# Optimization experiments

Measured on AMD Instinct MI355X. Metric: run time of the kernel, lower is better.

Reference implementation:

```python
import jax, jax.numpy as jnp
import numpy as np

N = 100000
E = 1600000
IN_C, HID_C, OUT_C = 64, 64, 16


def setup_inputs() -> dict:
    key = jax.random.key(0)
    k1, k2, k3, k4, k5 = jax.random.split(key, 5)
    x = jax.random.normal(k1, (N, IN_C), dtype=jnp.float32)
    edge_index = jax.random.randint(k2, (2, E), 0, N, dtype=jnp.int64)
    # Glorot-style init like PyG GCNConv
    W1 = jax.random.normal(k3, (IN_C, HID_C), dtype=jnp.float32) * (1.0 / np.sqrt(IN_C))
    b1 = jnp.zeros((HID_C,), dtype=jnp.float32)
    W2 = jax.random.normal(k4, (HID_C, OUT_C), dtype=jnp.float32) * (1.0 / np.sqrt(HID_C))
    b2 = jnp.zeros((OUT_C,), dtype=jnp.float32)
    return {"x": x, "edge_index": edge_index, "W1": W1, "b1": b1, "W2": W2, "b2": b2}


def _gcn_conv(h, src, dst, norm, W, b, n_nodes):
    # h: [N, F_in] -> linear transform first (PyG order), then normalized aggregation
    h = h @ W  # [N, F_out]
    msgs = h[src] * norm[:, None]          # gather + scale, [E+N, F_out]
    out = jax.ops.segment_sum(msgs, dst, num_segments=n_nodes)  # scatter-add
    return out + b


def reference(x, edge_index, W1, b1, W2, b2):
    n = x.shape[0]
    loop = jnp.arange(n, dtype=edge_index.dtype)
    src = jnp.concatenate([edge_index[0], loop])  # add self-loops
    dst = jnp.concatenate([edge_index[1], loop])
    # symmetric normalization D^{-1/2} (A+I) D^{-1/2}
    deg = jax.ops.segment_sum(jnp.ones_like(dst, dtype=x.dtype), dst, num_segments=n)
    dinv = jnp.where(deg > 0, jax.lax.rsqrt(deg), 0.0)
    norm = dinv[src] * dinv[dst]  # [E+N]

    h = jax.nn.relu(_gcn_conv(x, src, dst, norm, W1, b1, n))
    # dropout is identity in eval mode
    return _gcn_conv(h, src, dst, norm, W2, b2, n)
```

## Files before the change

kernel.cpp:

```cpp
#include <hip/hip_runtime.h>


namespace {
constexpr int BLK = 256;
constexpr int NPB = 256;
constexpr int PCHUNK = 8192;
constexpr int STRIDE = 5120;
constexpr int CPAD = 32;

__device__ inline float bf2f(unsigned short h) {
    union { unsigned u; float f; } v; v.u = (unsigned)h << 16; return v.f;
}
__device__ inline unsigned short f2bf(float f) {
    union { float f; unsigned u; } v; v.f = f;
    unsigned r = (v.u + 0x7FFFu + ((v.u >> 16) & 1u)) >> 16;
    return (unsigned short)r;
}
__device__ inline unsigned pack2bf(float a, float b) {
    return (unsigned)f2bf(a) | ((unsigned)f2bf(b) << 16);
}
__device__ inline int sel4(int s0, int s1, int s2, int s3, int q) {
    int sa = (q & 1) ? s1 : s0;
    int sb = (q & 1) ? s3 : s2;
    return (q & 2) ? sb : sa;
}

__device__ inline float gather8(const unsigned short* __restrict__ hhat,
                                const int* __restrict__ ssrc,
                                const float* __restrict__ dinv,
                                int base, int lane) {
    int s0 = ssrc[base + 0], s1 = ssrc[base + 1];
    int s2 = ssrc[base + 2], s3 = ssrc[base + 3];
    int s4 = ssrc[base + 4], s5 = ssrc[base + 5];
    int s6 = ssrc[base + 6], s7 = ssrc[base + 7];
    float d0 = dinv[s0], d1 = dinv[s1], d2 = dinv[s2], d3 = dinv[s3];
    float d4 = dinv[s4], d5 = dinv[s5], d6 = dinv[s6], d7 = dinv[s7];
    float v0 = bf2f(hhat[((size_t)s0 << 6) + lane]);
    float v1 = bf2f(hhat[((size_t)s1 << 6) + lane]);
    float v2 = bf2f(hhat[((size_t)s2 << 6) + lane]);
    float v3 = bf2f(hhat[((size_t)s3 << 6) + lane]);
    float v4 = bf2f(hhat[((size_t)s4 << 6) + lane]);
    float v5 = bf2f(hhat[((size_t)s5 << 6) + lane]);
    float v6 = bf2f(hhat[((size_t)s6 << 6) + lane]);
    float v7 = bf2f(hhat[((size_t)s7 << 6) + lane]);
    float t0 = fmaf(d1, v1, d0 * v0);
    float t1 = fmaf(d3, v3, d2 * v2);
    float t2 = fmaf(d5, v5, d4 * v4);
    float t3 = fmaf(d7, v7, d6 * v6);
    return (t0 + t1) + (t2 + t3);
}
__device__ inline float gather4(const unsigned short* __restrict__ hhat,
                                const int* __restrict__ ssrc,
                                const float* __restrict__ dinv,
                                int base, int lane) {
    int s0 = ssrc[base + 0], s1 = ssrc[base + 1];
    int s2 = ssrc[base + 2], s3 = ssrc[base + 3];
    float d0 = dinv[s0], d1 = dinv[s1], d2 = dinv[s2], d3 = dinv[s3];
    float v0 = bf2f(hhat[((size_t)s0 << 6) + lane]);
    float v1 = bf2f(hhat[((size_t)s1 << 6) + lane]);
    float v2 = bf2f(hhat[((size_t)s2 << 6) + lane]);
    float v3 = bf2f(hhat[((size_t)s3 << 6) + lane]);
    float t0 = fmaf(d1, v1, d0 * v0);
    float t1 = fmaf(d3, v3, d2 * v2);
    return t0 + t1;
}

__global__ __launch_bounds__(BLK) void k_part(const int* __restrict__ src,
                                              const int* __restrict__ dst,
                                              int* __restrict__ bcnt,
                                              unsigned* __restrict__ packed,
                                              int e, int nb) {
    __shared__ int hist[1024];
    __shared__ int base[1024];
    int t = threadIdx.x;
    int chunk0 = blockIdx.x * PCHUNK;
    if (chunk0 >= e) return;
    int lim = min(PCHUNK, e - chunk0);
    int lim4 = lim >> 2;
    for (int i = t; i < nb; i += BLK) hist[i] = 0;
    __syncthreads();
    const int4* d4 = (const int4*)(dst + chunk0);
    for (int i = t; i < lim4; i += BLK) {
        int4 d = d4[i];
        atomicAdd(&hist[d.x >> 8], 1);
        atomicAdd(&hist[d.y >> 8], 1);
        atomicAdd(&hist[d.z >> 8], 1);
        atomicAdd(&hist[d.w >> 8], 1);
    }
    for (int i = (lim4 << 2) + t; i < lim; i += BLK)
        atomicAdd(&hist[dst[chunk0 + i] >> 8], 1);
    __syncthreads();
    for (int i = t; i < nb; i += BLK) {
        int c = hist[i];
        base[i] = c ? (i * STRIDE + atomicAdd(&bcnt[i * CPAD], c)) : 0;
        hist[i] = 0;
    }
    __syncthreads();
    const int4* s4 = (const int4*)(src + chunk0);
    for (int i = t; i < lim4; i += BLK) {
        int4 d = d4[i];
        int4 s = s4[i];
        int b0 = d.x >> 8, b1 = d.y >> 8, b2 = d.z >> 8, b3 = d.w >> 8;
        int r0 = atomicAdd(&hist[b0], 1);
        packed[base[b0] + r0] = ((unsigned)s.x << 8) | (unsigned)(d.x & 255);
        int r1 = atomicAdd(&hist[b1], 1);
        packed[base[b1] + r1] = ((unsigned)s.y << 8) | (unsigned)(d.y & 255);
        int r2 = atomicAdd(&hist[b2], 1);
        packed[base[b2] + r2] = ((unsigned)s.z << 8) | (unsigned)(d.z & 255);
        int r3 = atomicAdd(&hist[b3], 1);
        packed[base[b3] + r3] = ((unsigned)s.w << 8) | (unsigned)(d.w & 255);
    }
    for (int i = (lim4 << 2) + t; i < lim; i += BLK) {
        int d = dst[chunk0 + i];
        int b = d >> 8;
        int r = atomicAdd(&hist[b], 1);
        packed[base[b] + r] = ((unsigned)src[chunk0 + i] << 8) | (unsigned)(d & 255);
    }
}

union SMemU {
    struct { unsigned sp[STRIDE]; int cnt[NPB]; int offs[NPB]; } s;
    float W[64 * 64];
};

__global__ __launch_bounds__(BLK) void k_sortgemm(
    const unsigned* __restrict__ packed, const int* __restrict__ bcnt,
    int* __restrict__ ssrc, int* __restrict__ rowbeg, int* __restrict__ rowcnt,
    float* __restrict__ dinv, int n, int nsort,
    const float* __restrict__ x, const float* __restrict__ W1,
    unsigned short* __restrict__ hhat, int ntiles) {
    __shared__ SMemU sm;
    int t = threadIdx.x;
    if ((int)blockIdx.x < nsort) {
        int bid = blockIdx.x;
        int b = bid >> 2;
        int qr = bid & 3;
        int regionBase = b * STRIDE;
        int ecnt = bcnt[b * CPAD];
        sm.s.cnt[t] = 0;
        __syncthreads();
        for (int i = t; i < ecnt; i += BLK) {
            unsigned p = packed[regionBase + i];
            sm.s.sp[i] = p;
            atomicAdd(&sm.s.cnt[p & 255u], 1);
        }
        __syncthreads();
        int v = sm.s.cnt[t];
        sm.s.offs[t] = v;
        __syncthreads();
        for (int off = 1; off < NPB; off <<= 1) {
            int xx = (t >= off) ? sm.s.offs[t - off] : 0;
            __syncthreads();
            sm.s.offs[t] += xx;
            __syncthreads();
        }
        int myoff = sm.s.offs[t] - v;
        int node = (b << 8) + t;
        if ((t >> 6) == qr && node < n) {
            rowbeg[node] = regionBase + myoff;
            rowcnt[node] = v;
            dinv[node] = rsqrtf((float)(v + 1));
        }
        __syncthreads();
        sm.s.cnt[t] = regionBase + myoff;
        __syncthreads();
        int lo = qr << 6, hi = lo + 64;
        for (int i = t; i < ecnt; i += BLK) {
            unsigned p = sm.s.sp[i];
            int dl = (int)(p & 255u);
            if (dl >= lo && dl < hi) {
                int pos = atomicAdd(&sm.s.cnt[dl], 1);
                ssrc[pos] = (int)(p >> 8);
            }
        }
    } else {
        #pragma unroll
        for (int i = 0; i < 16; ++i) sm.W[t + BLK * i] = W1[t + BLK * i];
        __syncthreads();
        const int cg = t & 3;
        const int ng = t >> 2;
        const float* Wc = sm.W + cg * 16;
        const int g1grid = gridDim.x - nsort;

        for (int tile = blockIdx.x - nsort; tile < ntiles; tile += g1grid) {
            const int node0 = tile * 256 + ng * 4;
            int nd[4];
            #pragma unroll
            for (int i = 0; i < 4; ++i) {
                int vv = node0 + i;
                nd[i] = (vv < n) ? vv : (n - 1);
            }
            float4 acc[4][4];
            #pragma unroll
            for (int i = 0; i < 4; ++i)
                #pragma unroll
                for (int c = 0; c < 4; ++c) acc[i][c] = make_float4(0.f, 0.f, 0.f, 0.f);

            for (int k4 = 0; k4 < 16; ++k4) {
                float4 xv[4];
                #pragma unroll
                for (int i = 0; i < 4; ++i)
                    xv[i] = ((const float4*)(x + (size_t)nd[i] * 64))[k4];
                #pragma unroll
                for (int kk = 0; kk < 4; ++kk) {
                    const float4* wr = (const float4*)(Wc + (k4 * 4 + kk) * 64);
                    float4 w0 = wr[0], w1 = wr[1], w2 = wr[2], w3 = wr[3];
                    #pragma unroll
                    for (int i = 0; i < 4; ++i) {
                        float xa[4] = {xv[i].x, xv[i].y, xv[i].z, xv[i].w};
                        float xs = xa[kk];
                        acc[i][0].x = fmaf(xs, w0.x, acc[i][0].x);
                        acc[i][0].y = fmaf(xs, w0.y, acc[i][0].y);
                        acc[i][0].z = fmaf(xs, w0.z, acc[i][0].z);
                        acc[i][0].w = fmaf(xs, w0.w, acc[i][0].w);
                        acc[i][1].x = fmaf(xs, w1.x, acc[i][1].x);
                        acc[i][1].y = fmaf(xs, w1.y, acc[i][1].y);
                        acc[i][1].z = fmaf(xs, w1.z, acc[i][1].z);
                        acc[i][1].w = fmaf(xs, w1.w, acc[i][1].w);
                        acc[i][2].x = fmaf(xs, w2.x, acc[i][2].x);
                        acc[i][2].y = fmaf(xs, w2.y, acc[i][2].y);
                        acc[i][2].z = fmaf(xs, w2.z, acc[i][2].z);
                        acc[i][2].w = fmaf(xs, w2.w, acc[i][2].w);
                        acc[i][3].x = fmaf(xs, w3.x, acc[i][3].x);
                        acc[i][3].y = fmaf(xs, w3.y, acc[i][3].y);
                        acc[i][3].z = fmaf(xs, w3.z, acc[i][3].z);
                        acc[i][3].w = fmaf(xs, w3.w, acc[i][3].w);
                    }
                }
            }
            #pragma unroll
            for (int i = 0; i < 4; ++i) {
                int vv = node0 + i;
                if (vv < n) {
                    unsigned u0 = pack2bf(acc[i][0].x, acc[i][0].y);
                    unsigned u1 = pack2bf(acc[i][0].z, acc[i][0].w);
                    unsigned u2 = pack2bf(acc[i][1].x, acc[i][1].y);
                    unsigned u3 = pack2bf(acc[i][1].z, acc[i][1].w);
                    unsigned u4 = pack2bf(acc[i][2].x, acc[i][2].y);
                    unsigned u5 = pack2bf(acc[i][2].z, acc[i][2].w);
                    unsigned u6 = pack2bf(acc[i][3].x, acc[i][3].y);
                    unsigned u7 = pack2bf(acc[i][3].z, acc[i][3].w);
                    uint4* dstp = (uint4*)(hhat + (size_t)vv * 64 + cg * 16);
                    dstp[0] = make_uint4(u0, u1, u2, u3);
                    dstp[1] = make_uint4(u4, u5, u6, u7);
                }
            }
        }
    }
}


__global__ __launch_bounds__(BLK) void k_agg1(const unsigned short* __restrict__ hhat,
                                              const int* __restrict__ rowbeg,
                                              const int* __restrict__ rowcnt,
                                              const int* __restrict__ ssrc,
                                              const float* __restrict__ dinv,
                                              const float* __restrict__ b1,
                                              const float* __restrict__ W2,
                                              unsigned short* __restrict__ h2hat, int n) {
    int pair = __builtin_amdgcn_readfirstlane(
        (int)((blockIdx.x * BLK + threadIdx.x) >> 6));
    int lane = threadIdx.x & 63;
    int wid0 = pair << 1;
    if (wid0 >= n) return;
    int wid1 = wid0 + 1;
    bool has1 = (wid1 < n);
    const int g = lane >> 4;
    const int j = lane & 15;
    float w2r[16];
    #pragma unroll
    for (int k = 0; k < 16; ++k) w2r[k] = W2[(g * 16 + k) * 16 + j];

    int beg0 = rowbeg[wid0], cnt0 = rowcnt[wid0];
    int beg1 = 0, cnt1 = 0;
    if (has1) { beg1 = rowbeg[wid1]; cnt1 = rowcnt[wid1]; }
    float a0 = dinv[wid0] * bf2f(hhat[((size_t)wid0 << 6) + lane]);
    float a1 = 0.f;
    if (has1) a1 = dinv[wid1] * bf2f(hhat[((size_t)wid1 << 6) + lane]);
    int e0 = 0, e1 = 0;
    while (e0 + 8 <= cnt0 && e1 + 8 <= cnt1) {
        float r0 = gather8(hhat, ssrc, dinv, beg0 + e0, lane);
        float r1 = gather8(hhat, ssrc, dinv, beg1 + e1, lane);
        a0 += r0;
        a1 += r1;
        e0 += 8; e1 += 8;
    }
    for (; e0 + 8 <= cnt0; e0 += 8) a0 += gather8(hhat, ssrc, dinv, beg0 + e0, lane);
    for (; e1 + 8 <= cnt1; e1 += 8) a1 += gather8(hhat, ssrc, dinv, beg1 + e1, lane);
    if (e0 + 4 <= cnt0) { a0 += gather4(hhat, ssrc, dinv, beg0 + e0, lane); e0 += 4; }
    if (e1 + 4 <= cnt1) { a1 += gather4(hhat, ssrc, dinv, beg1 + e1, lane); e1 += 4; }
    for (; e0 < cnt0; ++e0) {
        int s = ssrc[beg0 + e0];
        a0 = fmaf(dinv[s], bf2f(hhat[((size_t)s << 6) + lane]), a0);
    }
    for (; e1 < cnt1; ++e1) {
        int s = ssrc[beg1 + e1];
        a1 = fmaf(dinv[s], bf2f(hhat[((size_t)s << 6) + lane]), a1);
    }

    {
        float dv = dinv[wid0];
        float h = fmaxf(fmaf(dv, a0, b1[lane]), 0.f);
        float part = 0.f;
        #pragma unroll
        for (int k = 0; k < 16; ++k)
            part = fmaf(__shfl(h, g * 16 + k, 64), w2r[k], part);
        part += __shfl_xor(part, 16, 64);
        part += __shfl_xor(part, 32, 64);
        if (g == 0) h2hat[(size_t)wid0 * 16 + j] = f2bf(part * dv);
    }
    if (has1) {
        float dv = dinv[wid1];
        float h = fmaxf(fmaf(dv, a1, b1[lane]), 0.f);
        float part = 0.f;
        #pragma unroll
        for (int k = 0; k < 16; ++k)
            part = fmaf(__shfl(h, g * 16 + k, 64), w2r[k], part);
        part += __shfl_xor(part, 16, 64);
        part += __shfl_xor(part, 32, 64);
        if (g == 0) h2hat[(size_t)wid1 * 16 + j] = f2bf(part * dv);
    }
}

__global__ __launch_bounds__(BLK) void k_agg2(const unsigned short* __restrict__ h2,
                                              const int* __restrict__ rowbeg,
                                              const int* __restrict__ rowcnt,
                                              const int* __restrict__ ssrc,
                                              const float* __restrict__ dinv,
                                              const float* __restrict__ b2,
                                              float* __restrict__ out, int n) {
    int pair = __builtin_amdgcn_readfirstlane(
        (int)((blockIdx.x * BLK + threadIdx.x) >> 6));
    int lane = threadIdx.x & 63;
    int w0 = pair << 1;
    if (w0 >= n) return;
    int w1 = w0 + 1;
    bool has1 = (w1 < n);
    int q = lane >> 4;
    int c = lane & 15;
    int beg0 = rowbeg[w0], cnt0 = rowcnt[w0];
    int beg1 = 0, cnt1 = 0;
    if (has1) { beg1 = rowbeg[w1]; cnt1 = rowcnt[w1]; }
    float a0 = 0.f, a1 = 0.f;
    int e0 = 0, e1 = 0;
    while (e0 + 8 <= cnt0 && e1 + 8 <= cnt1) {
        int p0 = beg0 + e0, p1 = beg1 + e1;
        int x0 = ssrc[p0 + 0], x1 = ssrc[p0 + 1], x2 = ssrc[p0 + 2], x3 = ssrc[p0 + 3];
        int x4 = ssrc[p0 + 4], x5 = ssrc[p0 + 5], x6 = ssrc[p0 + 6], x7 = ssrc[p0 + 7];
        int y0 = ssrc[p1 + 0], y1 = ssrc[p1 + 1], y2 = ssrc[p1 + 2], y3 = ssrc[p1 + 3];
        int y4 = ssrc[p1 + 4], y5 = ssrc[p1 + 5], y6 = ssrc[p1 + 6], y7 = ssrc[p1 + 7];
        int sA0 = sel4(x0, x1, x2, x3, q), sB0 = sel4(x4, x5, x6, x7, q);
        int sA1 = sel4(y0, y1, y2, y3, q), sB1 = sel4(y4, y5, y6, y7, q);
        float vA0 = bf2f(h2[((size_t)sA0 << 4) + c]);
        float vB0 = bf2f(h2[((size_t)sB0 << 4) + c]);
        float vA1 = bf2f(h2[((size_t)sA1 << 4) + c]);
        float vB1 = bf2f(h2[((size_t)sB1 << 4) + c]);
        a0 += vA0 + vB0;
        a1 += vA1 + vB1;
        e0 += 8; e1 += 8;
    }
    for (; e0 + 8 <= cnt0; e0 += 8) {
        int p0 = beg0 + e0;
        int x0 = ssrc[p0 + 0], x1 = ssrc[p0 + 1], x2 = ssrc[p0 + 2], x3 = ssrc[p0 + 3];
        int x4 = ssrc[p0 + 4], x5 = ssrc[p0 + 5], x6 = ssrc[p0 + 6], x7 = ssrc[p0 + 7];
        int sA = sel4(x0, x1, x2, x3, q), sB = sel4(x4, x5, x6, x7, q);
        a0 += bf2f(h2[((size_t)sA << 4) + c]) + bf2f(h2[((size_t)sB << 4) + c]);
    }
    if (e0 + 4 <= cnt0) {
        int p0 = beg0 + e0;
        int x0 = ssrc[p0 + 0], x1 = ssrc[p0 + 1], x2 = ssrc[p0 + 2], x3 = ssrc[p0 + 3];
        a0 += bf2f(h2[((size_t)sel4(x0, x1, x2, x3, q) << 4) + c]);
        e0 += 4;
    }
    if (e0 + q < cnt0)
        a0 += bf2f(h2[((size_t)ssrc[beg0 + e0 + q] << 4) + c]);
    for (; e1 + 8 <= cnt1; e1 += 8) {
        int p1 = beg1 + e1;
        int y0 = ssrc[p1 + 0], y1 = ssrc[p1 + 1], y2 = ssrc[p1 + 2], y3 = ssrc[p1 + 3];
        int y4 = ssrc[p1 + 4], y5 = ssrc[p1 + 5], y6 = ssrc[p1 + 6], y7 = ssrc[p1 + 7];
        int sA = sel4(y0, y1, y2, y3, q), sB = sel4(y4, y5, y6, y7, q);
        a1 += bf2f(h2[((size_t)sA << 4) + c]) + bf2f(h2[((size_t)sB << 4) + c]);
    }
    if (has1 && e1 + 4 <= cnt1) {
        int p1 = beg1 + e1;
        int y0 = ssrc[p1 + 0], y1 = ssrc[p1 + 1], y2 = ssrc[p1 + 2], y3 = ssrc[p1 + 3];
        a1 += bf2f(h2[((size_t)sel4(y0, y1, y2, y3, q) << 4) + c]);
        e1 += 4;
    }
    if (has1 && e1 + q < cnt1)
        a1 += bf2f(h2[((size_t)ssrc[beg1 + e1 + q] << 4) + c]);

    a0 += __shfl_xor(a0, 16, 64);
    a0 += __shfl_xor(a0, 32, 64);
    a1 += __shfl_xor(a1, 16, 64);
    a1 += __shfl_xor(a1, 32, 64);
    if (q == 0) {
        float self0 = bf2f(h2[((size_t)w0 << 4) + c]);
        out[((size_t)w0 << 4) + c] = fmaf(dinv[w0], a0 + self0, b2[c]);
        if (has1) {
            float self1 = bf2f(h2[((size_t)w1 << 4) + c]);
            out[((size_t)w1 << 4) + c] = fmaf(dinv[w1], a1 + self1, b2[c]);
        }
    }
}

}

extern "C" void kernel_launch(void* const* d_in, const int* in_sizes, int n_in,
                              void* d_out, int out_size, void* d_ws, size_t ws_size,
                              hipStream_t stream) {
    const float* x  = (const float*)d_in[0];
    const int*   ei = (const int*)d_in[1];
    const float* W1 = (const float*)d_in[2];
    const float* b1 = (const float*)d_in[3];
    const float* W2 = (const float*)d_in[4];
    const float* b2 = (const float*)d_in[5];
    float* out = (float*)d_out;

    const int N = in_sizes[0] / 64;
    const int E = in_sizes[1] / 2;
    const int* src = ei;
    const int* dst = ei + E;
    const int nb = (N + NPB - 1) / NPB;

    char* ws = (char*)d_ws;
    size_t off = 0;
    auto alloc = [&](size_t bytes) -> char* {
        char* p = ws + off;
        off = (off + bytes + 255) & ~(size_t)255;
        return p;
    };
    int*            bcnt   = (int*)alloc((size_t)1024 * CPAD * 4);
    int*            rowbeg = (int*)alloc((size_t)N * 4);
    int*            rowcnt = (int*)alloc((size_t)N * 4);
    float*          dinv   = (float*)alloc((size_t)N * 4);
    unsigned*       packed = (unsigned*)alloc((size_t)nb * STRIDE * 4);
    int*            ssrc   = (int*)alloc((size_t)nb * STRIDE * 4);
    unsigned short* hhat   = (unsigned short*)alloc((size_t)N * 64 * 2);
    unsigned short* h2hat  = (unsigned short*)alloc((size_t)N * 16 * 2);

    const int ntiles = (N + 255) / 256;
    const int g1grid = (ntiles < 1024) ? ntiles : 1024;
    const int nchunks = (E + PCHUNK - 1) / PCHUNK;
    const int npairs = (N + 1) / 2;
    const int nb_p = (int)(((long long)npairs * 64 + BLK - 1) / BLK);
    const int nsort = nb * 4;

    const int zn = nb * CPAD;
    hipMemsetAsync(bcnt, 0, (size_t)zn * 4, stream);
    k_part<<<nchunks, BLK, 0, stream>>>(src, dst, bcnt, packed, E, nb);
    k_sortgemm<<<nsort + g1grid, BLK, 0, stream>>>(packed, bcnt, ssrc, rowbeg,
                                                   rowcnt, dinv, N, nsort,
                                                   x, W1, hhat, ntiles);
    k_agg1<<<nb_p, BLK, 0, stream>>>(hhat, rowbeg, rowcnt, ssrc, dinv, b1, W2,
                                     h2hat, N);
    k_agg2<<<nb_p, BLK, 0, stream>>>(h2hat, rowbeg, rowcnt, ssrc, dinv, b2, out, N);
}
```

Before: 217.9 us.

## Prescale layer-1 features by source dinv to drop per-edge dinv gathers

Computes node in-degrees with global atomics during partitioning, so the GEMM stage can fold dinv[src] into the bf16 hhat rows before they are stored. Layer-1 aggregation then becomes a plain sum of gathered rows, with no per-edge random dinv load and multiply. The cost is an extra global atomic per edge in k_part and a larger memset, and dinv is now applied before bf16 rounding, which slightly changes numerics. The GEMM blocks share a launch with the sort blocks, so deg must be complete before that launch.

```diff
diff --git a/kernel.cpp b/kernel.cpp
--- a/kernel.cpp
+++ b/kernel.cpp
@@ -26,15 +26,11 @@
 }
 
 __device__ inline float gather8(const unsigned short* __restrict__ hhat,
-                                const int* __restrict__ ssrc,
-                                const float* __restrict__ dinv,
-                                int base, int lane) {
+                                const int* __restrict__ ssrc, int base, int lane) {
     int s0 = ssrc[base + 0], s1 = ssrc[base + 1];
     int s2 = ssrc[base + 2], s3 = ssrc[base + 3];
     int s4 = ssrc[base + 4], s5 = ssrc[base + 5];
     int s6 = ssrc[base + 6], s7 = ssrc[base + 7];
-    float d0 = dinv[s0], d1 = dinv[s1], d2 = dinv[s2], d3 = dinv[s3];
-    float d4 = dinv[s4], d5 = dinv[s5], d6 = dinv[s6], d7 = dinv[s7];
     float v0 = bf2f(hhat[((size_t)s0 << 6) + lane]);
     float v1 = bf2f(hhat[((size_t)s1 << 6) + lane]);
     float v2 = bf2f(hhat[((size_t)s2 << 6) + lane]);
@@ -43,31 +39,23 @@
     float v5 = bf2f(hhat[((size_t)s5 << 6) + lane]);
     float v6 = bf2f(hhat[((size_t)s6 << 6) + lane]);
     float v7 = bf2f(hhat[((size_t)s7 << 6) + lane]);
-    float t0 = fmaf(d1, v1, d0 * v0);
-    float t1 = fmaf(d3, v3, d2 * v2);
-    float t2 = fmaf(d5, v5, d4 * v4);
-    float t3 = fmaf(d7, v7, d6 * v6);
-    return (t0 + t1) + (t2 + t3);
+    return ((v0 + v1) + (v2 + v3)) + ((v4 + v5) + (v6 + v7));
 }
 __device__ inline float gather4(const unsigned short* __restrict__ hhat,
-                                const int* __restrict__ ssrc,
-                                const float* __restrict__ dinv,
-                                int base, int lane) {
+                                const int* __restrict__ ssrc, int base, int lane) {
     int s0 = ssrc[base + 0], s1 = ssrc[base + 1];
     int s2 = ssrc[base + 2], s3 = ssrc[base + 3];
-    float d0 = dinv[s0], d1 = dinv[s1], d2 = dinv[s2], d3 = dinv[s3];
     float v0 = bf2f(hhat[((size_t)s0 << 6) + lane]);
     float v1 = bf2f(hhat[((size_t)s1 << 6) + lane]);
     float v2 = bf2f(hhat[((size_t)s2 << 6) + lane]);
     float v3 = bf2f(hhat[((size_t)s3 << 6) + lane]);
-    float t0 = fmaf(d1, v1, d0 * v0);
-    float t1 = fmaf(d3, v3, d2 * v2);
-    return t0 + t1;
+    return (v0 + v1) + (v2 + v3);
 }
 
 __global__ __launch_bounds__(BLK) void k_part(const int* __restrict__ src,
                                               const int* __restrict__ dst,
                                               int* __restrict__ bcnt,
+                                              int* __restrict__ deg,
                                               unsigned* __restrict__ packed,
                                               int e, int nb) {
     __shared__ int hist[1024];
@@ -86,9 +74,16 @@
         atomicAdd(&hist[d.y >> 8], 1);
         atomicAdd(&hist[d.z >> 8], 1);
         atomicAdd(&hist[d.w >> 8], 1);
-    }
-    for (int i = (lim4 << 2) + t; i < lim; i += BLK)
-        atomicAdd(&hist[dst[chunk0 + i] >> 8], 1);
+        atomicAdd(&deg[d.x], 1);
+        atomicAdd(&deg[d.y], 1);
+        atomicAdd(&deg[d.z], 1);
+        atomicAdd(&deg[d.w], 1);
+    }
+    for (int i = (lim4 << 2) + t; i < lim; i += BLK) {
+        int d = dst[chunk0 + i];
+        atomicAdd(&hist[d >> 8], 1);
+        atomicAdd(&deg[d], 1);
+    }
     __syncthreads();
     for (int i = t; i < nb; i += BLK) {
         int c = hist[i];
@@ -128,6 +123,7 @@
     int* __restrict__ ssrc, int* __restrict__ rowbeg, int* __restrict__ rowcnt,
     float* __restrict__ dinv, int n, int nsort,
     const float* __restrict__ x, const float* __restrict__ W1,
+    const int* __restrict__ deg,
     unsigned short* __restrict__ hhat, int ntiles) {
     __shared__ SMemU sm;
     int t = threadIdx.x;
@@ -232,14 +228,15 @@
             for (int i = 0; i < 4; ++i) {
                 int vv = node0 + i;
                 if (vv < n) {
-                    unsigned u0 = pack2bf(acc[i][0].x, acc[i][0].y);
-                    unsigned u1 = pack2bf(acc[i][0].z, acc[i][0].w);
-                    unsigned u2 = pack2bf(acc[i][1].x, acc[i][1].y);
-                    unsigned u3 = pack2bf(acc[i][1].z, acc[i][1].w);
-                    unsigned u4 = pack2bf(acc[i][2].x, acc[i][2].y);
-                    unsigned u5 = pack2bf(acc[i][2].z, acc[i][2].w);
-                    unsigned u6 = pack2bf(acc[i][3].x, acc[i][3].y);
-                    unsigned u7 = pack2bf(acc[i][3].z, acc[i][3].w);
+                    float d = rsqrtf((float)(deg[vv] + 1));
+                    unsigned u0 = pack2bf(acc[i][0].x * d, acc[i][0].y * d);
+                    unsigned u1 = pack2bf(acc[i][0].z * d, acc[i][0].w * d);
+                    unsigned u2 = pack2bf(acc[i][1].x * d, acc[i][1].y * d);
+                    unsigned u3 = pack2bf(acc[i][1].z * d, acc[i][1].w * d);
+                    unsigned u4 = pack2bf(acc[i][2].x * d, acc[i][2].y * d);
+                    unsigned u5 = pack2bf(acc[i][2].z * d, acc[i][2].w * d);
+                    unsigned u6 = pack2bf(acc[i][3].x * d, acc[i][3].y * d);
+                    unsigned u7 = pack2bf(acc[i][3].z * d, acc[i][3].w * d);
                     uint4* dstp = (uint4*)(hhat + (size_t)vv * 64 + cg * 16);
                     dstp[0] = make_uint4(u0, u1, u2, u3);
                     dstp[1] = make_uint4(u4, u5, u6, u7);
@@ -274,29 +271,23 @@
     int beg0 = rowbeg[wid0], cnt0 = rowcnt[wid0];
     int beg1 = 0, cnt1 = 0;
     if (has1) { beg1 = rowbeg[wid1]; cnt1 = rowcnt[wid1]; }
-    float a0 = dinv[wid0] * bf2f(hhat[((size_t)wid0 << 6) + lane]);
+    float a0 = bf2f(hhat[((size_t)wid0 << 6) + lane]);
     float a1 = 0.f;
-    if (has1) a1 = dinv[wid1] * bf2f(hhat[((size_t)wid1 << 6) + lane]);
+    if (has1) a1 = bf2f(hhat[((size_t)wid1 << 6) + lane]);
     int e0 = 0, e1 = 0;
     while (e0 + 8 <= cnt0 && e1 + 8 <= cnt1) {
-        float r0 = gather8(hhat, ssrc, dinv, beg0 + e0, lane);
-        float r1 = gather8(hhat, ssrc, dinv, beg1 + e1, lane);
+        float r0 = gather8(hhat, ssrc, beg0 + e0, lane);
+        float r1 = gather8(hhat, ssrc, beg1 + e1, lane);
         a0 += r0;
         a1 += r1;
         e0 += 8; e1 += 8;
     }
-    for (; e0 + 8 <= cnt0; e0 += 8) a0 += gather8(hhat, ssrc, dinv, beg0 + e0, lane);
-    for (; e1 + 8 <= cnt1; e1 += 8) a1 += gather8(hhat, ssrc, dinv, beg1 + e1, lane);
-    if (e0 + 4 <= cnt0) { a0 += gather4(hhat, ssrc, dinv, beg0 + e0, lane); e0 += 4; }
-    if (e1 + 4 <= cnt1) { a1 += gather4(hhat, ssrc, dinv, beg1 + e1, lane); e1 += 4; }
-    for (; e0 < cnt0; ++e0) {
-        int s = ssrc[beg0 + e0];
-        a0 = fmaf(dinv[s], bf2f(hhat[((size_t)s << 6) + lane]), a0);
-    }
-    for (; e1 < cnt1; ++e1) {
-        int s = ssrc[beg1 + e1];
-        a1 = fmaf(dinv[s], bf2f(hhat[((size_t)s << 6) + lane]), a1);
-    }
+    for (; e0 + 8 <= cnt0; e0 += 8) a0 += gather8(hhat, ssrc, beg0 + e0, lane);
+    for (; e1 + 8 <= cnt1; e1 += 8) a1 += gather8(hhat, ssrc, beg1 + e1, lane);
+    if (e0 + 4 <= cnt0) { a0 += gather4(hhat, ssrc, beg0 + e0, lane); e0 += 4; }
+    if (e1 + 4 <= cnt1) { a1 += gather4(hhat, ssrc, beg1 + e1, lane); e1 += 4; }
+    for (; e0 < cnt0; ++e0) a0 += bf2f(hhat[((size_t)ssrc[beg0 + e0] << 6) + lane]);
+    for (; e1 < cnt1; ++e1) a1 += bf2f(hhat[((size_t)ssrc[beg1 + e1] << 6) + lane]);
 
     {
         float dv = dinv[wid0];
@@ -431,6 +422,7 @@
         return p;
     };
     int*            bcnt   = (int*)alloc((size_t)1024 * CPAD * 4);
+    int*            deg    = (int*)alloc((size_t)N * 4);
     int*            rowbeg = (int*)alloc((size_t)N * 4);
     int*            rowcnt = (int*)alloc((size_t)N * 4);
     float*          dinv   = (float*)alloc((size_t)N * 4);
@@ -446,12 +438,11 @@
     const int nb_p = (int)(((long long)npairs * 64 + BLK - 1) / BLK);
     const int nsort = nb * 4;
 
-    const int zn = nb * CPAD;
-    hipMemsetAsync(bcnt, 0, (size_t)zn * 4, stream);
-    k_part<<<nchunks, BLK, 0, stream>>>(src, dst, bcnt, packed, E, nb);
+    hipMemsetAsync(bcnt, 0, (size_t)1024 * CPAD * 4 + ((size_t)N * 4 + 255 & ~(size_t)255), stream);
+    k_part<<<nchunks, BLK, 0, stream>>>(src, dst, bcnt, deg, packed, E, nb);
     k_sortgemm<<<nsort + g1grid, BLK, 0, stream>>>(packed, bcnt, ssrc, rowbeg,
                                                    rowcnt, dinv, N, nsort,
-                                                   x, W1, hhat, ntiles);
+                                                   x, W1, deg, hhat, ntiles);
     k_agg1<<<nb_p, BLK, 0, stream>>>(hhat, rowbeg, rowcnt, ssrc, dinv, b1, W2,
                                      h2hat, N);
     k_agg2<<<nb_p, BLK, 0, stream>>>(h2hat, rowbeg, rowcnt, ssrc, dinv, b2, out, N);
```

Result: slower. 267.9 us (+23.0%).
